# Kernel optimization log

Measured on AMD Instinct MI355X. Metric: run time of the kernel, lower is better.

## Reference

```python
import jax, jax.numpy as jnp
import numpy as np

N = 50000   # nodes
C = 64      # channels (in == out)
E = 800000  # edges (before self-loops)
EPS = 1e-5  # BatchNorm eps


def _bn(h, gamma, beta):
    # training-mode BatchNorm1d over the node (batch) axis
    mu = h.mean(0)
    var = h.var(0)
    return (h - mu) * jax.lax.rsqrt(var + EPS) * gamma + beta


def setup_inputs() -> dict:
    key = jax.random.key(0)
    ks = jax.random.split(key, 20)
    p = lambda i, shape, s=0.1: jax.random.normal(ks[i], shape, jnp.float32) * s
    src = jax.random.randint(ks[2], (E,), 0, N, dtype=jnp.int32)
    # guarantee no self-loops (PointTransformerConv removes then re-adds them)
    dst = (src + 1 + jax.random.randint(ks[3], (E,), 0, N - 1, dtype=jnp.int32)) % N
    return dict(
        x=p(0, (N, C), 1.0),
        pos=p(1, (N, 3), 1.0),
        edge_index=jnp.stack([src, dst]),
        Win=p(4, (C, C)), bin_=p(5, (C,)), gin=jnp.ones((C,), jnp.float32), betain=jnp.zeros((C,), jnp.float32),
        Wv=p(6, (C, C)), Wk=p(7, (C, C)), Wq=p(8, (C, C)),
        P1=p(9, (3, C)), pb1=p(10, (C,)), P2=p(11, (C, C)), pb2=p(12, (C,)),
        A1=p(13, (C, C)), ab1=p(14, (C,)), A2=p(15, (C, C)), ab2=p(16, (C,)),
        Wout=p(17, (C, C)), bout=p(18, (C,)), gout=jnp.ones((C,), jnp.float32), betaout=jnp.zeros((C,), jnp.float32),
    )


def reference(x, pos, edge_index, Win, bin_, gin, betain, Wv, Wk, Wq,
              P1, pb1, P2, pb2, A1, ab1, A2, ab2, Wout, bout, gout, betaout):
    silu = jax.nn.silu
    # mlp_in: Linear + BN + SiLU (plain_last=False)
    x = silu(_bn(x @ Win + bin_, gin, betain))

    # PointTransformerConv (add_self_loops=True)
    loop = jnp.arange(N, dtype=edge_index.dtype)
    src = jnp.concatenate([edge_index[0], loop])  # j
    dst = jnp.concatenate([edge_index[1], loop])  # i

    v = x @ Wv       # lin (values), bias=False
    k = x @ Wk       # lin_src
    q = x @ Wq       # lin_dst

    # per-edge positional encoding: pos_nn = SiLU(SiLU((pos_i - pos_j) P1 + b) P2 + b)
    delta = silu(silu((pos[dst] - pos[src]) @ P1 + pb1) @ P2 + pb2)  # [Etot, C]
    # attention logits: attn_nn(alpha_i - alpha_j + delta)
    alpha = q[dst] - k[src] + delta
    alpha = silu(silu(alpha @ A1 + ab1) @ A2 + ab2)

    # segment-wise (per-dst-node, per-channel) softmax over neighborhoods
    m = jax.ops.segment_max(alpha, dst, num_segments=N)
    ex = jnp.exp(alpha - m[dst])
    denom = jax.ops.segment_sum(ex, dst, num_segments=N)
    attn = ex / denom[dst]

    # weighted scatter-reduce of messages
    out = jax.ops.segment_sum(attn * (v[src] + delta), dst, num_segments=N)  # [N, C]

    # mlp_out: Linear + BN, act=None
    return _bn(out @ Wout + bout, gout, betaout)
```

## Files before the change

### kernel.cpp

```cpp
#include <hip/hip_runtime.h>

#define CH 64
#define BN_EPS 1e-5f

typedef __attribute__((ext_vector_type(8))) __bf16 bf16x8;
typedef __attribute__((ext_vector_type(4))) float f32x4;

__device__ __forceinline__ float silu_f(float x) { return x / (1.0f + __expf(-x)); }

__global__ __launch_bounds__(256) void k_lin_in(
    const float* __restrict__ x, const float* __restrict__ Win, const float* __restrict__ bin,
    float* __restrict__ h, float* __restrict__ ssum, float* __restrict__ ssq, int N)
{
    __shared__ float xt[64 * 64];
    __shared__ float Wl[64 * 64];
    __shared__ float red[2][4][64];
    const int t = threadIdx.x, c = t & 63, g = t >> 6;
    const int row0 = blockIdx.x * 64;

    for (int i = t; i < 64 * 64; i += 256) {
        int r = i >> 6, cc = i & 63;
        int gr = row0 + r;
        xt[i] = (gr < N) ? x[(size_t)gr * CH + cc] : 0.0f;
        Wl[i] = Win[i];
    }
    __syncthreads();

    float acc[16];
    const float b = bin[c];
#pragma unroll
    for (int i = 0; i < 16; ++i) acc[i] = b;
    for (int k = 0; k < 64; ++k) {
        float w = Wl[k * 64 + c];
#pragma unroll
        for (int i = 0; i < 16; ++i) acc[i] += xt[(g * 16 + i) * 64 + k] * w;
    }
    float s = 0.0f, ss = 0.0f;
#pragma unroll
    for (int i = 0; i < 16; ++i) {
        int gr = row0 + g * 16 + i;
        if (gr < N) {
            h[(size_t)gr * CH + c] = acc[i];
            s += acc[i];
            ss += acc[i] * acc[i];
        }
    }
    red[0][g][c] = s;
    red[1][g][c] = ss;
    __syncthreads();
    if (g == 0) {
        atomicAdd(&ssum[c], red[0][0][c] + red[0][1][c] + red[0][2][c] + red[0][3][c]);
        atomicAdd(&ssq[c],  red[1][0][c] + red[1][1][c] + red[1][2][c] + red[1][3][c]);
    }
}

__global__ void k_stats(const float* __restrict__ ssum, const float* __restrict__ ssq,
                        const float* __restrict__ gamma, const float* __restrict__ beta,
                        float* __restrict__ scale, float* __restrict__ shift, int N)
{
    int c = threadIdx.x;
    float inv = 1.0f / (float)N;
    float mu = ssum[c] * inv;
    float var = ssq[c] * inv - mu * mu;
    float sc = gamma[c] * rsqrtf(var + BN_EPS);
    scale[c] = sc;
    shift[c] = beta[c] - mu * sc;
}

__global__ __launch_bounds__(256) void k_vkq(
    const float* __restrict__ h, const float* __restrict__ scale, const float* __restrict__ shift,
    const float* __restrict__ Wv, const float* __restrict__ Wk, const float* __restrict__ Wq,
    __bf16* __restrict__ vv, __bf16* __restrict__ kk, __bf16* __restrict__ qq, int N)
{
    __shared__ float xt[64 * 64];
    __shared__ float Wl[2][64 * 64];
    const int t = threadIdx.x, c = t & 63, g = t >> 6;
    const int row0 = blockIdx.x * 64;

    for (int i = t; i < 64 * 64; i += 256) {
        int r = i >> 6, cc = i & 63;
        int gr = row0 + r;
        float hv = (gr < N) ? h[(size_t)gr * CH + cc] : 0.0f;
        xt[i] = silu_f(hv * scale[cc] + shift[cc]);
        Wl[0][i] = Wv[i];
        Wl[1][i] = Wk[i];
    }
    __syncthreads();

    for (int m = 0; m < 2; ++m) {
        float acc[16];
#pragma unroll
        for (int i = 0; i < 16; ++i) acc[i] = 0.0f;
        for (int k = 0; k < 64; ++k) {
            float w = Wl[m][k * 64 + c];
#pragma unroll
            for (int i = 0; i < 16; ++i) acc[i] += xt[(g * 16 + i) * 64 + k] * w;
        }
        __bf16* o = (m == 0) ? vv : kk;
#pragma unroll
        for (int i = 0; i < 16; ++i) {
            int gr = row0 + g * 16 + i;
            if (gr < N) o[(size_t)gr * CH + c] = (__bf16)acc[i];
        }
    }
    __syncthreads();
    for (int i = t; i < 64 * 64; i += 256) Wl[0][i] = Wq[i];
    __syncthreads();
    {
        float acc[16];
#pragma unroll
        for (int i = 0; i < 16; ++i) acc[i] = 0.0f;
        for (int k = 0; k < 64; ++k) {
            float w = Wl[0][k * 64 + c];
#pragma unroll
            for (int i = 0; i < 16; ++i) acc[i] += xt[(g * 16 + i) * 64 + k] * w;
        }
#pragma unroll
        for (int i = 0; i < 16; ++i) {
            int gr = row0 + g * 16 + i;
            if (gr < N) qq[(size_t)gr * CH + c] = (__bf16)acc[i];
        }
    }
}

__global__ __launch_bounds__(256) void k_edge_mfma(
    const int* __restrict__ srcA, const int* __restrict__ dstA,
    const float* __restrict__ pos,
    const __bf16* __restrict__ vvb, const __bf16* __restrict__ kkb, const __bf16* __restrict__ qqb,
    const float* __restrict__ P1, const float* __restrict__ pb1,
    const float* __restrict__ P2, const float* __restrict__ pb2,
    const float* __restrict__ A1, const float* __restrict__ ab1,
    const float* __restrict__ A2, const float* __restrict__ ab2,
    float* __restrict__ num, float* __restrict__ den,
    int E, int Etot, int nChunks)
{
    __shared__ __align__(16) __bf16 Wtab[3][8][64][8];
    __shared__ __align__(16) __bf16 tb[4][16][72];

    const int t = threadIdx.x;
    for (int i = t; i < 3 * 4096; i += 256) {
        int mat = i >> 12, r = i & 4095;
        int j = r & 7, lane = (r >> 3) & 63, ksnt = r >> 9;
        int ks = ksnt & 1, nt = ksnt >> 1;
        int k = ks * 32 + ((lane >> 4) & 3) * 8 + j;
        int n = nt * 16 + (lane & 15);
        const float* W = (mat == 0) ? P2 : ((mat == 1) ? A1 : A2);
        Wtab[mat][ksnt][lane][j] = (__bf16)W[k * 64 + n];
    }
    __syncthreads();

    const int l = t & 63, wid = t >> 6, lg = l >> 4, lm = l & 15;
    __bf16* tbw = &tb[wid][0][0];

    float pb1r[4], pb2r[4], ab1r[4], ab2r[4];
    bf16x8 p1f[4];
#pragma unroll
    for (int nt = 0; nt < 4; ++nt) {
        int co = nt * 16 + lm;
        pb1r[nt] = pb1[co]; pb2r[nt] = pb2[co];
        ab1r[nt] = ab1[co]; ab2r[nt] = ab2[co];
        bf16x8 f;
#pragma unroll
        for (int j = 0; j < 8; ++j)
            f[j] = (__bf16)((lg == 0 && j < 3) ? P1[j * 64 + co] : 0.0f);
        p1f[nt] = f;
    }

    int ch = blockIdx.x;
    if (ch >= nChunks) return;

    int sC = 0, dC = 0;
    {
        int eA = ch * 64 + wid * 16 + lm;
        if (eA < Etot) { if (eA < E) { sC = srcA[eA]; dC = dstA[eA]; } else { sC = dC = eA - E; } }
    }
    float pdl[3];
    bf16x8 qmk0, qmk1;
    {
        const float* ps = pos + (size_t)sC * 3;
        const float* pd = pos + (size_t)dC * 3;
        pdl[0] = pd[0] - ps[0]; pdl[1] = pd[1] - ps[1]; pdl[2] = pd[2] - ps[2];
        const __bf16* qp = qqb + (size_t)dC * 64 + lg * 8;
        const __bf16* kp = kkb + (size_t)sC * 64 + lg * 8;
        bf16x8 q0 = *(const bf16x8*)qp, q1 = *(const bf16x8*)(qp + 32);
        bf16x8 k0 = *(const bf16x8*)kp, k1 = *(const bf16x8*)(kp + 32);
#pragma unroll
        for (int j = 0; j < 8; ++j) {
            qmk0[j] = (__bf16)((float)q0[j] - (float)k0[j]);
            qmk1[j] = (__bf16)((float)q1[j] - (float)k1[j]);
        }
    }

    for (;;) {
        const int e0 = ch * 64 + wid * 16;
        const int chn = ch + gridDim.x;
        const bool hn = chn < nChunks;

        int sN = 0, dN = 0;
        if (hn) {
            int eA = chn * 64 + wid * 16 + lm;
            if (eA < Etot) { if (eA < E) { sN = srcA[eA]; dN = dstA[eA]; } else { sN = dN = eA - E; } }
        }

        int dD[4];
        __bf16 vpre[4][4];
#pragma unroll
        for (int jj = 0; jj < 4; ++jj) {
            int sD = __shfl(sC, lg * 4 + jj);
            dD[jj] = __shfl(dC, lg * 4 + jj);
            const __bf16* vp = vvb + (size_t)sD * 64 + lm;
#pragma unroll
            for (int nt = 0; nt < 4; ++nt) vpre[jj][nt] = vp[nt * 16];
        }

        bf16x8 af;
        af[0] = (lg == 0) ? (__bf16)pdl[0] : (__bf16)0.0f;
        af[1] = (lg == 0) ? (__bf16)pdl[1] : (__bf16)0.0f;
        af[2] = (lg == 0) ? (__bf16)pdl[2] : (__bf16)0.0f;
        af[3] = af[4] = af[5] = af[6] = af[7] = (__bf16)0.0f;
        f32x4 acc[4];
#pragma unroll
        for (int nt = 0; nt < 4; ++nt) {
            f32x4 a; a[0] = a[1] = a[2] = a[3] = pb1r[nt];
            acc[nt] = __builtin_amdgcn_mfma_f32_16x16x32_bf16(af, p1f[nt], a, 0, 0, 0);
        }
#pragma unroll
        for (int nt = 0; nt < 4; ++nt)
#pragma unroll
            for (int jj = 0; jj < 4; ++jj)
                tbw[(lg * 4 + jj) * 72 + nt * 16 + lm] = (__bf16)silu_f(acc[nt][jj]);
        bf16x8 aX0 = *(const bf16x8*)&tbw[lm * 72 + lg * 8];
        bf16x8 aX1 = *(const bf16x8*)&tbw[lm * 72 + 32 + lg * 8];

#pragma unroll
        for (int nt = 0; nt < 4; ++nt) {
            f32x4 a; a[0] = a[1] = a[2] = a[3] = pb2r[nt];
            a = __builtin_amdgcn_mfma_f32_16x16x32_bf16(aX0, *(const bf16x8*)&Wtab[0][nt * 2 + 0][l][0], a, 0, 0, 0);
            a = __builtin_amdgcn_mfma_f32_16x16x32_bf16(aX1, *(const bf16x8*)&Wtab[0][nt * 2 + 1][l][0], a, 0, 0, 0);
            acc[nt] = a;
        }
        float dlt[4][4];
#pragma unroll
        for (int nt = 0; nt < 4; ++nt)
#pragma unroll
            for (int jj = 0; jj < 4; ++jj) {
                float dv = silu_f(acc[nt][jj]);
                dlt[nt][jj] = dv;
                tbw[(lg * 4 + jj) * 72 + nt * 16 + lm] = (__bf16)dv;
            }

        float pdlN[3];
        bf16x8 qmkN0, qmkN1;
        if (hn) {
            const float* ps = pos + (size_t)sN * 3;
            const float* pd = pos + (size_t)dN * 3;
            pdlN[0] = pd[0] - ps[0]; pdlN[1] = pd[1] - ps[1]; pdlN[2] = pd[2] - ps[2];
            const __bf16* qp = qqb + (size_t)dN * 64 + lg * 8;
            const __bf16* kp = kkb + (size_t)sN * 64 + lg * 8;
            bf16x8 q0 = *(const bf16x8*)qp, q1 = *(const bf16x8*)(qp + 32);
            bf16x8 k0 = *(const bf16x8*)kp, k1 = *(const bf16x8*)(kp + 32);
#pragma unroll
            for (int j = 0; j < 8; ++j) {
                qmkN0[j] = (__bf16)((float)q0[j] - (float)k0[j]);
                qmkN1[j] = (__bf16)((float)q1[j] - (float)k1[j]);
            }
        }

        bf16x8 dA0 = *(const bf16x8*)&tbw[lm * 72 + lg * 8];
        bf16x8 dA1 = *(const bf16x8*)&tbw[lm * 72 + 32 + lg * 8];
        bf16x8 aA0, aA1;
#pragma unroll
        for (int j = 0; j < 8; ++j) {
            aA0[j] = (__bf16)((float)qmk0[j] + (float)dA0[j]);
            aA1[j] = (__bf16)((float)qmk1[j] + (float)dA1[j]);
        }

#pragma unroll
        for (int nt = 0; nt < 4; ++nt) {
            f32x4 a; a[0] = a[1] = a[2] = a[3] = ab1r[nt];
            a = __builtin_amdgcn_mfma_f32_16x16x32_bf16(aA0, *(const bf16x8*)&Wtab[1][nt * 2 + 0][l][0], a, 0, 0, 0);
            a = __builtin_amdgcn_mfma_f32_16x16x32_bf16(aA1, *(const bf16x8*)&Wtab[1][nt * 2 + 1][l][0], a, 0, 0, 0);
            acc[nt] = a;
        }
#pragma unroll
        for (int nt = 0; nt < 4; ++nt)
#pragma unroll
            for (int jj = 0; jj < 4; ++jj)
                tbw[(lg * 4 + jj) * 72 + nt * 16 + lm] = (__bf16)silu_f(acc[nt][jj]);
        bf16x8 aY0 = *(const bf16x8*)&tbw[lm * 72 + lg * 8];
        bf16x8 aY1 = *(const bf16x8*)&tbw[lm * 72 + 32 + lg * 8];

#pragma unroll
        for (int nt = 0; nt < 4; ++nt) {
            f32x4 a; a[0] = a[1] = a[2] = a[3] = ab2r[nt];
            a = __builtin_amdgcn_mfma_f32_16x16x32_bf16(aY0, *(const bf16x8*)&Wtab[2][nt * 2 + 0][l][0], a, 0, 0, 0);
            a = __builtin_amdgcn_mfma_f32_16x16x32_bf16(aY1, *(const bf16x8*)&Wtab[2][nt * 2 + 1][l][0], a, 0, 0, 0);
            acc[nt] = a;
        }

#pragma unroll
        for (int jj = 0; jj < 4; ++jj) {
            const int eD = e0 + lg * 4 + jj;
            if (eD < Etot) {
                const size_t ob = (size_t)dD[jj] * 64 + lm;
#pragma unroll
                for (int nt = 0; nt < 4; ++nt) {
                    float ex = __expf(silu_f(acc[nt][jj]));
                    atomicAdd(&den[ob + nt * 16], ex);
                    atomicAdd(&num[ob + nt * 16], ex * ((float)vpre[jj][nt] + dlt[nt][jj]));
                }
            }
        }

        if (!hn) break;
        sC = sN; dC = dN;
        pdl[0] = pdlN[0]; pdl[1] = pdlN[1]; pdl[2] = pdlN[2];
        qmk0 = qmkN0; qmk1 = qmkN1;
        ch = chn;
    }
}

__global__ __launch_bounds__(256) void k_out(
    const float* __restrict__ num, const float* __restrict__ den,
    const float* __restrict__ Wout, const float* __restrict__ bout,
    float* __restrict__ o, float* __restrict__ ssum, float* __restrict__ ssq, int N)
{
    __shared__ float xt[64 * 64];
    __shared__ float Wl[64 * 64];
    __shared__ float red[2][4][64];
    const int t = threadIdx.x, c = t & 63, g = t >> 6;
    const int row0 = blockIdx.x * 64;

    for (int i = t; i < 64 * 64; i += 256) {
        int r = i >> 6, cc = i & 63;
        int gr = row0 + r;
        xt[i] = (gr < N) ? num[(size_t)gr * CH + cc] / den[(size_t)gr * CH + cc] : 0.0f;
        Wl[i] = Wout[i];
    }
    __syncthreads();

    float acc[16];
    const float b = bout[c];
#pragma unroll
    for (int i = 0; i < 16; ++i) acc[i] = b;
    for (int k = 0; k < 64; ++k) {
        float w = Wl[k * 64 + c];
#pragma unroll
        for (int i = 0; i < 16; ++i) acc[i] += xt[(g * 16 + i) * 64 + k] * w;
    }
    float s = 0.0f, ss = 0.0f;
#pragma unroll
    for (int i = 0; i < 16; ++i) {
        int gr = row0 + g * 16 + i;
        if (gr < N) {
            o[(size_t)gr * CH + c] = acc[i];
            s += acc[i];
            ss += acc[i] * acc[i];
        }
    }
    red[0][g][c] = s;
    red[1][g][c] = ss;
    __syncthreads();
    if (g == 0) {
        atomicAdd(&ssum[c], red[0][0][c] + red[0][1][c] + red[0][2][c] + red[0][3][c]);
        atomicAdd(&ssq[c],  red[1][0][c] + red[1][1][c] + red[1][2][c] + red[1][3][c]);
    }
}

__global__ void k_final(const float* __restrict__ o, const float* __restrict__ scale,
                        const float* __restrict__ shift, float* __restrict__ out, int total)
{
    int i = blockIdx.x * blockDim.x + threadIdx.x;
    if (i < total) {
        int c = i & 63;
        out[i] = o[i] * scale[c] + shift[c];
    }
}

extern "C" void kernel_launch(void* const* d_in, const int* in_sizes, int n_in,
                              void* d_out, int out_size, void* d_ws, size_t ws_size,
                              hipStream_t stream)
{
    const float* x      = (const float*)d_in[0];
    const float* pos    = (const float*)d_in[1];
    const int*   ei     = (const int*)d_in[2];
    const float* Win    = (const float*)d_in[3];
    const float* bin    = (const float*)d_in[4];
    const float* gin    = (const float*)d_in[5];
    const float* betain = (const float*)d_in[6];
    const float* Wv     = (const float*)d_in[7];
    const float* Wk     = (const float*)d_in[8];
    const float* Wq     = (const float*)d_in[9];
    const float* P1     = (const float*)d_in[10];
    const float* pb1    = (const float*)d_in[11];
    const float* P2     = (const float*)d_in[12];
    const float* pb2    = (const float*)d_in[13];
    const float* A1     = (const float*)d_in[14];
    const float* ab1    = (const float*)d_in[15];
    const float* A2     = (const float*)d_in[16];
    const float* ab2    = (const float*)d_in[17];
    const float* Wout   = (const float*)d_in[18];
    const float* bout   = (const float*)d_in[19];
    const float* gout   = (const float*)d_in[20];
    const float* betaout= (const float*)d_in[21];

    const int N = in_sizes[0] / CH;
    const int E = in_sizes[2] / 2;
    const int Etot = E + N;
    const int* srcA = ei;
    const int* dstA = ei + E;

    float* ws = (float*)d_ws;
    const size_t NC = (size_t)N * CH;
    float* h    = ws;
    float* num  = h + NC;
    float* den  = num + NC;
    float* st   = den + NC;
    __bf16* vvb = (__bf16*)(st + 512);
    __bf16* kkb = vvb + NC;
    __bf16* qqb = kkb + NC;

    hipMemsetAsync(num, 0, (2 * NC + 512) * sizeof(float), stream);

    const int nb = (N + 63) / 64;
    k_lin_in<<<nb, 256, 0, stream>>>(x, Win, bin, h, st, st + 64, N);
    k_stats<<<1, 64, 0, stream>>>(st, st + 64, gin, betain, st + 128, st + 192, N);
    k_vkq<<<nb, 256, 0, stream>>>(h, st + 128, st + 192, Wv, Wk, Wq, vvb, kkb, qqb, N);

    const int nChunks = (Etot + 63) / 64;
    const int grid = (nChunks < 2048) ? nChunks : 2048;
    k_edge_mfma<<<grid, 256, 0, stream>>>(srcA, dstA, pos, vvb, kkb, qqb,
                                          P1, pb1, P2, pb2, A1, ab1, A2, ab2,
                                          num, den, E, Etot, nChunks);

    k_out<<<nb, 256, 0, stream>>>(num, den, Wout, bout, h, st + 256, st + 320, N);
    k_stats<<<1, 64, 0, stream>>>(st + 256, st + 320, gout, betaout, st + 384, st + 448, N);
    k_final<<<(int)((NC + 255) / 256), 256, 0, stream>>>(h, st + 384, st + 448,
                                                         (float*)d_out, (int)NC);
}
```

Baseline: 513.5 us.

## Sort edges by destination and merge same-destination atomics in edge kernel

Adds a counting sort of the edges by destination node: a histogram, a three-stage prefix scan and a scatter. The edge kernel then walks the sorted edge list. Within each lane's group of four consecutive edges, contributions to the same destination are summed in registers before being issued as atomics, which cuts the number of global atomicAdds and improves write locality. The cost is five extra kernel launches, more than a million atomic scatter operations, and extra workspace for the sorted arrays. Source-side gathers of v, k and pos also become more random.

```diff
diff --git a/kernel.cpp b/kernel.cpp
--- a/kernel.cpp
+++ b/kernel.cpp
@@ -123,8 +123,82 @@
     }
 }
 
+__global__ void k_hist(const int* __restrict__ dstA, int* __restrict__ cnt, int E, int Etot)
+{
+    int e = blockIdx.x * blockDim.x + threadIdx.x;
+    if (e < Etot) {
+        int d = (e < E) ? dstA[e] : (e - E);
+        atomicAdd(&cnt[d], 1);
+    }
+}
+
+__global__ __launch_bounds__(256) void k_scan_a(
+    const int* __restrict__ cnt, int* __restrict__ exc, int* __restrict__ bsum, int N)
+{
+    __shared__ int sh[256];
+    const int b = blockIdx.x, t = threadIdx.x;
+    const int base = b * 1024 + t * 4;
+    int v0 = (base + 0 < N) ? cnt[base + 0] : 0;
+    int v1 = (base + 1 < N) ? cnt[base + 1] : 0;
+    int v2 = (base + 2 < N) ? cnt[base + 2] : 0;
+    int v3 = (base + 3 < N) ? cnt[base + 3] : 0;
+    int s = v0 + v1 + v2 + v3;
+    sh[t] = s;
+    __syncthreads();
+    for (int off = 1; off < 256; off <<= 1) {
+        int x = (t >= off) ? sh[t - off] : 0;
+        __syncthreads();
+        sh[t] += x;
+        __syncthreads();
+    }
+    int p = sh[t] - s;
+    if (t == 255) bsum[b] = sh[255];
+    if (base + 0 < N) exc[base + 0] = p; p += v0;
+    if (base + 1 < N) exc[base + 1] = p; p += v1;
+    if (base + 2 < N) exc[base + 2] = p; p += v2;
+    if (base + 3 < N) exc[base + 3] = p;
+}
+
+__global__ __launch_bounds__(256) void k_scan_b(int* __restrict__ bsum, int nb)
+{
+    __shared__ int sh[256];
+    const int t = threadIdx.x;
+    int v = (t < nb) ? bsum[t] : 0;
+    sh[t] = v;
+    __syncthreads();
+    for (int off = 1; off < 256; off <<= 1) {
+        int x = (t >= off) ? sh[t - off] : 0;
+        __syncthreads();
+        sh[t] += x;
+        __syncthreads();
+    }
+    if (t < nb) bsum[t] = sh[t] - v;
+}
+
+__global__ void k_scan_c(const int* __restrict__ exc, const int* __restrict__ bsum,
+                         int* __restrict__ cur, int N)
+{
+    int i = blockIdx.x * blockDim.x + threadIdx.x;
+    if (i < N) cur[i] = exc[i] + bsum[i >> 10];
+}
+
+__global__ void k_scatter(const int* __restrict__ srcA, const int* __restrict__ dstA,
+                          int* __restrict__ cur, int* __restrict__ sortedS,
+                          int* __restrict__ sortedD, int E, int Etot)
+{
+    int e = blockIdx.x * blockDim.x + threadIdx.x;
+    if (e < Etot) {
+        int d, s;
+        if (e < E) { d = dstA[e]; s = srcA[e]; }
+        else       { d = s = e - E; }
+        int p = atomicAdd(&cur[d], 1);
+        sortedS[p] = s;
+        sortedD[p] = d;
+    }
+}
+
 __global__ __launch_bounds__(256) void k_edge_mfma(
-    const int* __restrict__ srcA, const int* __restrict__ dstA,
+    const int* __restrict__ sortedS, const int* __restrict__ sortedD,
     const float* __restrict__ pos,
     const __bf16* __restrict__ vvb, const __bf16* __restrict__ kkb, const __bf16* __restrict__ qqb,
     const float* __restrict__ P1, const float* __restrict__ pb1,
@@ -132,7 +206,7 @@
     const float* __restrict__ A1, const float* __restrict__ ab1,
     const float* __restrict__ A2, const float* __restrict__ ab2,
     float* __restrict__ num, float* __restrict__ den,
-    int E, int Etot, int nChunks)
+    int Etot, int nChunks)
 {
     __shared__ __align__(16) __bf16 Wtab[3][8][64][8];
     __shared__ __align__(16) __bf16 tb[4][16][72];
@@ -172,7 +246,7 @@
     int sC = 0, dC = 0;
     {
         int eA = ch * 64 + wid * 16 + lm;
-        if (eA < Etot) { if (eA < E) { sC = srcA[eA]; dC = dstA[eA]; } else { sC = dC = eA - E; } }
+        if (eA < Etot) { sC = sortedS[eA]; dC = sortedD[eA]; }
     }
     float pdl[3];
     bf16x8 qmk0, qmk1;
@@ -199,7 +273,7 @@
         int sN = 0, dN = 0;
         if (hn) {
             int eA = chn * 64 + wid * 16 + lm;
-            if (eA < Etot) { if (eA < E) { sN = srcA[eA]; dN = dstA[eA]; } else { sN = dN = eA - E; } }
+            if (eA < Etot) { sN = sortedS[eA]; dN = sortedD[eA]; }
         }
 
         int dD[4];
@@ -298,17 +372,36 @@
             acc[nt] = a;
         }
 
-#pragma unroll
-        for (int jj = 0; jj < 4; ++jj) {
-            const int eD = e0 + lg * 4 + jj;
-            if (eD < Etot) {
-                const size_t ob = (size_t)dD[jj] * 64 + lm;
+        {
+            float ad[4] = {0.f, 0.f, 0.f, 0.f};
+            float an[4] = {0.f, 0.f, 0.f, 0.f};
+            int curd = dD[0];
+#pragma unroll
+            for (int jj = 0; jj < 4; ++jj) {
+                const int eD = e0 + lg * 4 + jj;
+                const bool v = eD < Etot;
+                if (dD[jj] != curd) {
+                    const size_t ob = (size_t)curd * 64 + lm;
+#pragma unroll
+                    for (int nt = 0; nt < 4; ++nt) {
+                        atomicAdd(&den[ob + nt * 16], ad[nt]);
+                        atomicAdd(&num[ob + nt * 16], an[nt]);
+                        ad[nt] = 0.f; an[nt] = 0.f;
+                    }
+                    curd = dD[jj];
+                }
 #pragma unroll
                 for (int nt = 0; nt < 4; ++nt) {
-                    float ex = __expf(silu_f(acc[nt][jj]));
-                    atomicAdd(&den[ob + nt * 16], ex);
-                    atomicAdd(&num[ob + nt * 16], ex * ((float)vpre[jj][nt] + dlt[nt][jj]));
+                    float ex = v ? __expf(silu_f(acc[nt][jj])) : 0.0f;
+                    ad[nt] += ex;
+                    an[nt] += ex * ((float)vpre[jj][nt] + dlt[nt][jj]);
                 }
+            }
+            const size_t ob = (size_t)curd * 64 + lm;
+#pragma unroll
+            for (int nt = 0; nt < 4; ++nt) {
+                atomicAdd(&den[ob + nt * 16], ad[nt]);
+                atomicAdd(&num[ob + nt * 16], an[nt]);
             }
         }
 
@@ -416,11 +509,24 @@
     float* num  = h + NC;
     float* den  = num + NC;
     float* st   = den + NC;
-    __bf16* vvb = (__bf16*)(st + 512);
+    int* cnt    = (int*)(st + 512);
+    int* exc    = cnt + N;
+    int* cur    = exc + N;
+    int* bsum   = cur + N;
+    int* sortedS= bsum + 256;
+    int* sortedD= sortedS + Etot;
+    __bf16* vvb = (__bf16*)(sortedD + Etot);
     __bf16* kkb = vvb + NC;
     __bf16* qqb = kkb + NC;
 
-    hipMemsetAsync(num, 0, (2 * NC + 512) * sizeof(float), stream);
+    hipMemsetAsync(num, 0, (2 * NC + 512 + (size_t)N) * sizeof(float), stream);
+
+    const int nbScan = (N + 1023) / 1024;
+    k_hist<<<(Etot + 255) / 256, 256, 0, stream>>>(dstA, cnt, E, Etot);
+    k_scan_a<<<nbScan, 256, 0, stream>>>(cnt, exc, bsum, N);
+    k_scan_b<<<1, 256, 0, stream>>>(bsum, nbScan);
+    k_scan_c<<<(N + 255) / 256, 256, 0, stream>>>(exc, bsum, cur, N);
+    k_scatter<<<(Etot + 255) / 256, 256, 0, stream>>>(srcA, dstA, cur, sortedS, sortedD, E, Etot);
 
     const int nb = (N + 63) / 64;
     k_lin_in<<<nb, 256, 0, stream>>>(x, Win, bin, h, st, st + 64, N);
@@ -429,9 +535,9 @@
 
     const int nChunks = (Etot + 63) / 64;
     const int grid = (nChunks < 2048) ? nChunks : 2048;
-    k_edge_mfma<<<grid, 256, 0, stream>>>(srcA, dstA, pos, vvb, kkb, qqb,
+    k_edge_mfma<<<grid, 256, 0, stream>>>(sortedS, sortedD, pos, vvb, kkb, qqb,
                                           P1, pb1, P2, pb2, A1, ab1, A2, ab2,
-                                          num, den, E, Etot, nChunks);
+                                          num, den, Etot, nChunks);
 
     k_out<<<nb, 256, 0, stream>>>(num, den, Wout, bout, h, st + 256, st + 320, N);
     k_stats<<<1, 64, 0, stream>>>(st + 256, st + 320, gout, betaout, st + 384, st + 448, N);
```

After: 571.4 us. +11.3%, slower.

## Deepen edge-kernel prefetch pipeline and pad LDS transpose buffer to 66

Applied to the files above, without the earlier changes.

The edge kernel now gathers the value rows one iteration ahead and loads edge indices two chunks ahead, so gather latency overlaps the MFMA chain of the current chunk. The LDS transpose row stride drops from 72 to 66 bf16 to change the bank mapping. A launch-bounds occupancy hint of 4 is added and the persistent grid is halved to 1024 blocks. Atomics for out-of-range edges now run unconditionally with a zero contribution. The 66-element stride makes the 16-byte vector LDS reads misaligned for odd rows, which may split those accesses, and the extra prefetched registers could hurt occupancy.

```diff
diff --git a/kernel.cpp b/kernel.cpp
--- a/kernel.cpp
+++ b/kernel.cpp
@@ -123,7 +123,7 @@
     }
 }
 
-__global__ __launch_bounds__(256) void k_edge_mfma(
+__global__ __launch_bounds__(256, 4) void k_edge_mfma(
     const int* __restrict__ srcA, const int* __restrict__ dstA,
     const float* __restrict__ pos,
     const __bf16* __restrict__ vvb, const __bf16* __restrict__ kkb, const __bf16* __restrict__ qqb,
@@ -135,7 +135,7 @@
     int E, int Etot, int nChunks)
 {
     __shared__ __align__(16) __bf16 Wtab[3][8][64][8];
-    __shared__ __align__(16) __bf16 tb[4][16][72];
+    __shared__ __align__(16) __bf16 tb[4][16][66];
 
     const int t = threadIdx.x;
     for (int i = t; i < 3 * 4096; i += 256) {
@@ -166,6 +166,7 @@
         p1f[nt] = f;
     }
 
+    const int stride = gridDim.x;
     int ch = blockIdx.x;
     if (ch >= nChunks) return;
 
@@ -174,12 +175,12 @@
         int eA = ch * 64 + wid * 16 + lm;
         if (eA < Etot) { if (eA < E) { sC = srcA[eA]; dC = dstA[eA]; } else { sC = dC = eA - E; } }
     }
-    float pdl[3];
+    float pdl0, pdl1, pdl2;
     bf16x8 qmk0, qmk1;
     {
         const float* ps = pos + (size_t)sC * 3;
         const float* pd = pos + (size_t)dC * 3;
-        pdl[0] = pd[0] - ps[0]; pdl[1] = pd[1] - ps[1]; pdl[2] = pd[2] - ps[2];
+        pdl0 = pd[0] - ps[0]; pdl1 = pd[1] - ps[1]; pdl2 = pd[2] - ps[2];
         const __bf16* qp = qqb + (size_t)dC * 64 + lg * 8;
         const __bf16* kp = kkb + (size_t)sC * 64 + lg * 8;
         bf16x8 q0 = *(const bf16x8*)qp, q1 = *(const bf16x8*)(qp + 32);
@@ -190,33 +191,29 @@
             qmk1[j] = (__bf16)((float)q1[j] - (float)k1[j]);
         }
     }
+    __bf16 vcur[4][4];
+#pragma unroll
+    for (int jj = 0; jj < 4; ++jj) {
+        int sD = __shfl(sC, lg * 4 + jj);
+        const __bf16* vp = vvb + (size_t)sD * 64 + lm;
+#pragma unroll
+        for (int nt = 0; nt < 4; ++nt) vcur[jj][nt] = vp[nt * 16];
+    }
+    int chn = ch + stride;
+    bool hn = chn < nChunks;
+    int sN = 0, dN = 0;
+    if (hn) {
+        int eA = chn * 64 + wid * 16 + lm;
+        if (eA < Etot) { if (eA < E) { sN = srcA[eA]; dN = dstA[eA]; } else { sN = dN = eA - E; } }
+    }
 
     for (;;) {
         const int e0 = ch * 64 + wid * 16;
-        const int chn = ch + gridDim.x;
-        const bool hn = chn < nChunks;
-
-        int sN = 0, dN = 0;
-        if (hn) {
-            int eA = chn * 64 + wid * 16 + lm;
-            if (eA < Etot) { if (eA < E) { sN = srcA[eA]; dN = dstA[eA]; } else { sN = dN = eA - E; } }
-        }
-
-        int dD[4];
-        __bf16 vpre[4][4];
-#pragma unroll
-        for (int jj = 0; jj < 4; ++jj) {
-            int sD = __shfl(sC, lg * 4 + jj);
-            dD[jj] = __shfl(dC, lg * 4 + jj);
-            const __bf16* vp = vvb + (size_t)sD * 64 + lm;
-#pragma unroll
-            for (int nt = 0; nt < 4; ++nt) vpre[jj][nt] = vp[nt * 16];
-        }
 
         bf16x8 af;
-        af[0] = (lg == 0) ? (__bf16)pdl[0] : (__bf16)0.0f;
-        af[1] = (lg == 0) ? (__bf16)pdl[1] : (__bf16)0.0f;
-        af[2] = (lg == 0) ? (__bf16)pdl[2] : (__bf16)0.0f;
+        af[0] = (lg == 0) ? (__bf16)pdl0 : (__bf16)0.0f;
+        af[1] = (lg == 0) ? (__bf16)pdl1 : (__bf16)0.0f;
+        af[2] = (lg == 0) ? (__bf16)pdl2 : (__bf16)0.0f;
         af[3] = af[4] = af[5] = af[6] = af[7] = (__bf16)0.0f;
         f32x4 acc[4];
 #pragma unroll
@@ -228,9 +225,9 @@
         for (int nt = 0; nt < 4; ++nt)
 #pragma unroll
             for (int jj = 0; jj < 4; ++jj)
-                tbw[(lg * 4 + jj) * 72 + nt * 16 + lm] = (__bf16)silu_f(acc[nt][jj]);
-        bf16x8 aX0 = *(const bf16x8*)&tbw[lm * 72 + lg * 8];
-        bf16x8 aX1 = *(const bf16x8*)&tbw[lm * 72 + 32 + lg * 8];
+                tbw[(lg * 4 + jj) * 66 + nt * 16 + lm] = (__bf16)silu_f(acc[nt][jj]);
+        bf16x8 aX0 = *(const bf16x8*)&tbw[lm * 66 + lg * 8];
+        bf16x8 aX1 = *(const bf16x8*)&tbw[lm * 66 + 32 + lg * 8];
 
 #pragma unroll
         for (int nt = 0; nt < 4; ++nt) {
@@ -246,15 +243,16 @@
             for (int jj = 0; jj < 4; ++jj) {
                 float dv = silu_f(acc[nt][jj]);
                 dlt[nt][jj] = dv;
-                tbw[(lg * 4 + jj) * 72 + nt * 16 + lm] = (__bf16)dv;
+                tbw[(lg * 4 + jj) * 66 + nt * 16 + lm] = (__bf16)dv;
             }
 
-        float pdlN[3];
+        float pdlN0, pdlN1, pdlN2;
         bf16x8 qmkN0, qmkN1;
+        __bf16 vN[4][4];
         if (hn) {
             const float* ps = pos + (size_t)sN * 3;
             const float* pd = pos + (size_t)dN * 3;
-            pdlN[0] = pd[0] - ps[0]; pdlN[1] = pd[1] - ps[1]; pdlN[2] = pd[2] - ps[2];
+            pdlN0 = pd[0] - ps[0]; pdlN1 = pd[1] - ps[1]; pdlN2 = pd[2] - ps[2];
             const __bf16* qp = qqb + (size_t)dN * 64 + lg * 8;
             const __bf16* kp = kkb + (size_t)sN * 64 + lg * 8;
             bf16x8 q0 = *(const bf16x8*)qp, q1 = *(const bf16x8*)(qp + 32);
@@ -264,10 +262,25 @@
                 qmkN0[j] = (__bf16)((float)q0[j] - (float)k0[j]);
                 qmkN1[j] = (__bf16)((float)q1[j] - (float)k1[j]);
             }
-        }
-
-        bf16x8 dA0 = *(const bf16x8*)&tbw[lm * 72 + lg * 8];
-        bf16x8 dA1 = *(const bf16x8*)&tbw[lm * 72 + 32 + lg * 8];
+#pragma unroll
+            for (int jj = 0; jj < 4; ++jj) {
+                int sD = __shfl(sN, lg * 4 + jj);
+                const __bf16* vp = vvb + (size_t)sD * 64 + lm;
+#pragma unroll
+                for (int nt = 0; nt < 4; ++nt) vN[jj][nt] = vp[nt * 16];
+            }
+        }
+
+        const int chn2 = chn + stride;
+        const bool hn2 = hn && (chn2 < nChunks);
+        int sNN = 0, dNN = 0;
+        if (hn2) {
+            int eA = chn2 * 64 + wid * 16 + lm;
+            if (eA < Etot) { if (eA < E) { sNN = srcA[eA]; dNN = dstA[eA]; } else { sNN = dNN = eA - E; } }
+        }
+
+        bf16x8 dA0 = *(const bf16x8*)&tbw[lm * 66 + lg * 8];
+        bf16x8 dA1 = *(const bf16x8*)&tbw[lm * 66 + 32 + lg * 8];
         bf16x8 aA0, aA1;
 #pragma unroll
         for (int j = 0; j < 8; ++j) {
@@ -286,9 +299,9 @@
         for (int nt = 0; nt < 4; ++nt)
 #pragma unroll
             for (int jj = 0; jj < 4; ++jj)
-                tbw[(lg * 4 + jj) * 72 + nt * 16 + lm] = (__bf16)silu_f(acc[nt][jj]);
-        bf16x8 aY0 = *(const bf16x8*)&tbw[lm * 72 + lg * 8];
-        bf16x8 aY1 = *(const bf16x8*)&tbw[lm * 72 + 32 + lg * 8];
+                tbw[(lg * 4 + jj) * 66 + nt * 16 + lm] = (__bf16)silu_f(acc[nt][jj]);
+        bf16x8 aY0 = *(const bf16x8*)&tbw[lm * 66 + lg * 8];
+        bf16x8 aY1 = *(const bf16x8*)&tbw[lm * 66 + 32 + lg * 8];
 
 #pragma unroll
         for (int nt = 0; nt < 4; ++nt) {
@@ -301,22 +314,26 @@
 #pragma unroll
         for (int jj = 0; jj < 4; ++jj) {
             const int eD = e0 + lg * 4 + jj;
-            if (eD < Etot) {
-                const size_t ob = (size_t)dD[jj] * 64 + lm;
-#pragma unroll
-                for (int nt = 0; nt < 4; ++nt) {
-                    float ex = __expf(silu_f(acc[nt][jj]));
-                    atomicAdd(&den[ob + nt * 16], ex);
-                    atomicAdd(&num[ob + nt * 16], ex * ((float)vpre[jj][nt] + dlt[nt][jj]));
-                }
+            const bool v = eD < Etot;
+            const int dD = __shfl(dC, lg * 4 + jj);
+            const size_t ob = (size_t)dD * 64 + lm;
+#pragma unroll
+            for (int nt = 0; nt < 4; ++nt) {
+                float ex = v ? __expf(silu_f(acc[nt][jj])) : 0.0f;
+                atomicAdd(&den[ob + nt * 16], ex);
+                atomicAdd(&num[ob + nt * 16], ex * ((float)vcur[jj][nt] + dlt[nt][jj]));
             }
         }
 
         if (!hn) break;
-        sC = sN; dC = dN;
-        pdl[0] = pdlN[0]; pdl[1] = pdlN[1]; pdl[2] = pdlN[2];
+        ch = chn; chn = chn2; hn = hn2;
+        sC = sN; dC = dN; sN = sNN; dN = dNN;
+        pdl0 = pdlN0; pdl1 = pdlN1; pdl2 = pdlN2;
         qmk0 = qmkN0; qmk1 = qmkN1;
-        ch = chn;
+#pragma unroll
+        for (int jj = 0; jj < 4; ++jj)
+#pragma unroll
+            for (int nt = 0; nt < 4; ++nt) vcur[jj][nt] = vN[jj][nt];
     }
 }
 
@@ -428,7 +445,7 @@
     k_vkq<<<nb, 256, 0, stream>>>(h, st + 128, st + 192, Wv, Wk, Wq, vvb, kkb, qqb, N);
 
     const int nChunks = (Etot + 63) / 64;
-    const int grid = (nChunks < 2048) ? nChunks : 2048;
+    const int grid = (nChunks < 1024) ? nChunks : 1024;
     k_edge_mfma<<<grid, 256, 0, stream>>>(srcA, dstA, pos, vvb, kkb, qqb,
                                           P1, pb1, P2, pb2, A1, ab1, A2, ab2,
                                           num, den, E, Etot, nChunks);
```

After: 580.1 us. +13.0%, slower.
